# Performance work log

Hardware: AMD Instinct MI355X
Metric: run time of the kernel (lower is better)

Reference implementation:

```python
import jax, jax.numpy as jnp
import numpy as np

N = 100000   # nodes
E = 1600000  # edges (before self loops)
H = 4        # heads
C = 32       # per-head channels
D = H * C    # hidden_dim = 128
G = 64       # graphs in batch
L = 4        # num_layers
IN_DIM = 7
NEG_SLOPE = 0.2


def setup_inputs() -> dict:
    key = jax.random.key(0)
    ks = jax.random.split(key, 14)
    s = 0.1
    x = jax.random.normal(ks[0], (N, IN_DIM), jnp.float32)
    edge_index = jax.random.randint(ks[1], (2, E), 0, N, dtype=jnp.int32)
    batch = jnp.sort(jax.random.randint(ks[2], (N,), 0, G, dtype=jnp.int32))
    W0 = jax.random.normal(ks[3], (IN_DIM, D), jnp.float32) * s
    a_src0 = jax.random.normal(ks[4], (H, C), jnp.float32) * s
    a_dst0 = jax.random.normal(ks[5], (H, C), jnp.float32) * s
    b0 = jnp.zeros((D,), jnp.float32)
    Ws = jax.random.normal(ks[6], (L - 1, D, D), jnp.float32) * s
    a_srcs = jax.random.normal(ks[7], (L - 1, H, C), jnp.float32) * s
    a_dsts = jax.random.normal(ks[8], (L - 1, H, C), jnp.float32) * s
    bs = jnp.zeros((L - 1, D), jnp.float32)
    ln_g = jnp.ones((L, D), jnp.float32)
    ln_b = jnp.zeros((L, D), jnp.float32)
    return dict(x=x, edge_index=edge_index, batch=batch, W0=W0, a_src0=a_src0,
                a_dst0=a_dst0, b0=b0, Ws=Ws, a_srcs=a_srcs, a_dsts=a_dsts,
                bs=bs, ln_g=ln_g, ln_b=ln_b)


def _gat_layer(x, W, a_src, a_dst, b, src, dst):
    # x: [N, F_in] -> h: [N, H, C] (PyG GATConv: shared lin for src/dst)
    h = (x @ W).reshape(N, H, C)
    alpha_src = jnp.einsum('nhc,hc->nh', h, a_src)  # [N, H]
    alpha_dst = jnp.einsum('nhc,hc->nh', h, a_dst)  # [N, H]
    logits = jax.nn.leaky_relu(alpha_src[src] + alpha_dst[dst], NEG_SLOPE)  # [E', H]
    # segment softmax over edges grouped by destination node
    m = jax.ops.segment_max(logits, dst, num_segments=N)          # [N, H]
    e = jnp.exp(logits - m[dst])
    z = jax.ops.segment_sum(e, dst, num_segments=N)               # [N, H]
    alpha = e / (z[dst] + 1e-16)                                  # [E', H]
    msg = h[src] * alpha[..., None]                               # [E', H, C]
    out = jax.ops.segment_sum(msg, dst, num_segments=N)           # [N, H, C]
    return out.reshape(N, D) + b


def _layernorm(x, g, b):
    mu = jnp.mean(x, axis=-1, keepdims=True)
    var = jnp.var(x, axis=-1, keepdims=True)
    return (x - mu) * jax.lax.rsqrt(var + 1e-5) * g + b


def reference(x, edge_index, batch, W0, a_src0, a_dst0, b0, Ws, a_srcs, a_dsts, bs, ln_g, ln_b):
    # PyG GATConv default: add self loops
    loop = jnp.arange(N, dtype=edge_index.dtype)
    src = jnp.concatenate([edge_index[0], loop])
    dst = jnp.concatenate([edge_index[1], loop])
    h = x
    for i in range(L):
        if i == 0:
            W, asr, ads, b = W0, a_src0, a_dst0, b0
        else:
            W, asr, ads, b = Ws[i - 1], a_srcs[i - 1], a_dsts[i - 1], bs[i - 1]
        h_new = _gat_layer(h, W, asr, ads, b, src, dst)
        h_new = jax.nn.elu(_layernorm(h_new, ln_g[i], ln_b[i]))
        h = h + h_new if i > 0 else h_new  # dropout is identity in eval
    node_embeddings = h  # [N, D]
    sums = jax.ops.segment_sum(node_embeddings, batch, num_segments=G)  # [G, D]
    cnt = jax.ops.segment_sum(jnp.ones((N,), node_embeddings.dtype), batch, num_segments=G)
    graph_embedding = sums / jnp.maximum(cnt, 1.0)[:, None]
    return node_embeddings, graph_embedding
```

## Files before the change

### kernel.cpp

```cpp
#include <hip/hip_runtime.h>
#include <hip/hip_bf16.h>

#define NN 100000
#define NE 1600000
#define NH 4
#define NC 32
#define DD 128
#define NG 64
#define NIN 7

#define BSH 9
#define NBUK ((NN + 511) >> BSH)
#define SEGCAP 9600
#define CAPE (SEGCAP - 512)
#define CSRN (NBUK * SEGCAP)
#define NBBIN ((NE + 4095)/4096)

typedef __hip_bfloat16 bf16;
typedef __attribute__((ext_vector_type(8))) short short8;
typedef __attribute__((ext_vector_type(4))) float f32x4;
typedef __attribute__((ext_vector_type(2))) float f32x2;

__device__ __forceinline__ float b2f(const bf16 v){ return __bfloat162float(v); }

__device__ __forceinline__ float in_ld(const void* p, size_t i, int f32){
  return f32 ? ((const float*)p)[i] : b2f(((const bf16*)p)[i]);
}

__device__ __forceinline__ unsigned int bfbits(float v){
  bf16 b = __float2bfloat16(v);
  return (unsigned int)(*(unsigned short*)&b);
}

__global__ __launch_bounds__(256) void k_init(float* __restrict__ gsum, int* __restrict__ gcnt,
                                              int* __restrict__ bcur,
                                              const unsigned int* __restrict__ xb, int* __restrict__ flag){
  int i = blockIdx.x*256 + threadIdx.x;
  if (i < NG*DD) gsum[i] = 0.f;
  if (i < NG) gcnt[i] = 0;
  if (i < NBUK) bcur[i] = i * CAPE;
  if (blockIdx.x == 0 && threadIdx.x < 64){
    int t = threadIdx.x;
    int pl = 0;
    for (int j = t; j < 512; j += 64){
      float v = __uint_as_float(xb[j]);
      float a = fabsf(v);
      if (v == v && a < 1e6f && a > 1e-10f) pl++;
    }
    #pragma unroll
    for (int off = 32; off > 0; off >>= 1) pl += __shfl_down(pl, off);
    if (t == 0) *flag = (pl >= 384) ? 1 : 0;
  }
}

__global__ __launch_bounds__(256) void k_bin(const int* __restrict__ src, const int* __restrict__ dst,
                                             int* __restrict__ bcur, int2* __restrict__ gstag,
                                             const void* __restrict__ Ws, bf16* __restrict__ WT,
                                             const int* __restrict__ flag){
  if (blockIdx.x >= NBBIN){
    int l = blockIdx.x - NBBIN;
    int f32 = *flag;
    for (int idx = threadIdx.x; idx < DD*DD; idx += 256){
      int n = idx >> 7, k = idx & 127;
      WT[(size_t)l*DD*DD + idx] = __float2bfloat16(in_ld(Ws, (size_t)l*DD*DD + (size_t)k*DD + n, f32));
    }
    return;
  }
  __shared__ int cnt[NBUK], pref[NBUK+1], place[NBUK], gbase[NBUK];
  __shared__ int2 pairs[4096];
  int tid = threadIdx.x;
  for (int b = tid; b < NBUK; b += 256){ cnt[b]=0; place[b]=0; }
  __syncthreads();
  int e0 = blockIdx.x*4096;
  int s[16], d[16];
  #pragma unroll
  for (int i=0;i<16;i++){
    int e = e0 + i*256 + tid;
    s[i] = 0; d[i] = -1;
    if (e < NE){
      unsigned int us = (unsigned int)src[e]; if (us >= NN) us = 0;
      unsigned int ud = (unsigned int)dst[e]; if (ud >= NN) ud = 0;
      s[i] = (int)us; d[i] = (int)ud;
      atomicAdd(&cnt[ud>>BSH], 1);
    }
  }
  __syncthreads();
  if (tid == 0){
    int run = 0;
    for (int b=0;b<NBUK;b++){ pref[b] = run; run += cnt[b]; }
    pref[NBUK] = run;
  }
  __syncthreads();
  for (int b = tid; b < NBUK; b += 256){
    if (cnt[b] > 0) gbase[b] = atomicAdd(&bcur[b], cnt[b]);
  }
  __syncthreads();
  #pragma unroll
  for (int i=0;i<16;i++){
    if (d[i] >= 0){
      int b = d[i]>>BSH;
      int lp = atomicAdd(&place[b],1);
      pairs[pref[b]+lp] = make_int2(s[i], d[i]);
    }
  }
  __syncthreads();
  int tot = pref[NBUK];
  for (int j = tid; j < tot; j += 256){
    int2 pr = pairs[j];
    int b = pr.y>>BSH;
    int gidx = gbase[b] + (j - pref[b]);
    if (gidx >= b*CAPE && gidx < (b+1)*CAPE) gstag[gidx] = pr;
  }
}

__global__ __launch_bounds__(256) void k_bucket(const int2* __restrict__ gstag,
                                                const int* __restrict__ bcur,
                                                int* __restrict__ csr,
                                                int* __restrict__ offs, int* __restrict__ oend){
  __shared__ int seg[SEGCAP];
  __shared__ int lcnt[512];
  __shared__ int loff[512];
  __shared__ int pscan[256];
  int b = blockIdx.x, tid = threadIdx.x;
  int nstart = b << BSH;
  int nend = min(nstart + 512, NN);
  int nloc = nend - nstart;
  int base = b * SEGCAP;
  int stbase = b * CAPE;
  int ecnt = bcur[b] - stbase;
  ecnt = max(0, min(ecnt, CAPE));
  lcnt[tid]     = (tid < nloc) ? 1 : 0;
  lcnt[tid+256] = (tid+256 < nloc) ? 1 : 0;
  __syncthreads();
  for (int j = tid; j < ecnt; j += 256){
    int2 pr = gstag[stbase + j];
    int ln = pr.y - nstart;
    if (ln < 0 || ln >= nloc) ln = 0;
    atomicAdd(&lcnt[ln], 1);
  }
  __syncthreads();
  int c0 = lcnt[2*tid], c1 = lcnt[2*tid+1];
  int pairsum = c0 + c1;
  pscan[tid] = pairsum;
  __syncthreads();
  for (int off=1; off<256; off<<=1){
    int a = (tid >= off) ? pscan[tid-off] : 0;
    __syncthreads();
    pscan[tid] += a;
    __syncthreads();
  }
  int pexcl = pscan[tid] - pairsum;
  loff[2*tid]   = pexcl;
  loff[2*tid+1] = pexcl + c0;
  __syncthreads();
  int segN = pscan[255];
  if (segN > SEGCAP) segN = SEGCAP;
  if (tid < nloc){
    offs[nstart + tid] = base + loff[tid];
    oend[nstart + tid] = base + loff[tid] + lcnt[tid];
  }
  if (tid + 256 < nloc){
    offs[nstart + tid + 256] = base + loff[tid+256];
    oend[nstart + tid + 256] = base + loff[tid+256] + lcnt[tid+256];
  }
  __syncthreads();
  if (tid < nloc){ int p = loff[tid]; if (p < SEGCAP) seg[p] = nstart + tid; lcnt[tid] = 1; }
  if (tid + 256 < nloc){ int p = loff[tid+256]; if (p < SEGCAP) seg[p] = nstart + tid + 256; lcnt[tid+256] = 1; }
  __syncthreads();
  for (int j = tid; j < ecnt; j += 256){
    int2 pr = gstag[stbase + j];
    int ln = pr.y - nstart;
    if (ln < 0 || ln >= nloc) ln = 0;
    int p = atomicAdd(&lcnt[ln], 1);
    int idx = loff[ln] + p;
    if (idx >= 0 && idx < SEGCAP) seg[idx] = pr.x;
  }
  __syncthreads();
  for (int j = tid; j < segN; j += 256) csr[base + j] = seg[j];
}

__device__ __forceinline__ void alpha_red(float acc, float was, float wad, int d, int n,
                                          float* __restrict__ asrc, float* __restrict__ adst){
  float ps = acc*was, pd = acc*wad;
  #pragma unroll
  for (int off=16; off>0; off>>=1){
    ps += __shfl_down(ps, off, 32);
    pd += __shfl_down(pd, off, 32);
  }
  if ((d & 31) == 0){
    asrc[n*NH + (d>>5)] = ps;
    adst[n*NH + (d>>5)] = pd;
  }
}

__global__ __launch_bounds__(128) void k_gemm0(const void* __restrict__ x, const void* __restrict__ W,
    const void* __restrict__ aws, const void* __restrict__ awd,
    bf16* __restrict__ hproj,
    float* __restrict__ asrc, float* __restrict__ adst, const int* __restrict__ flag){
  int f32 = *flag;
  __shared__ float xr[4][NIN];
  int d = threadIdx.x;
  int n0 = blockIdx.x*4;
  if (d < 4*NIN) xr[d/NIN][d%NIN] = in_ld(x, (size_t)n0*NIN + d, f32);
  __syncthreads();
  float a0=0,a1=0,a2=0,a3=0;
  #pragma unroll
  for (int k=0;k<NIN;k++){
    float w = in_ld(W, (size_t)k*DD + d, f32);
    a0 += xr[0][k]*w; a1 += xr[1][k]*w; a2 += xr[2][k]*w; a3 += xr[3][k]*w;
  }
  hproj[(size_t)(n0+0)*DD+d]=__float2bfloat16(a0);
  hproj[(size_t)(n0+1)*DD+d]=__float2bfloat16(a1);
  hproj[(size_t)(n0+2)*DD+d]=__float2bfloat16(a2);
  hproj[(size_t)(n0+3)*DD+d]=__float2bfloat16(a3);
  float was = in_ld(aws, d, f32), wad = in_ld(awd, d, f32);
  alpha_red(a0, was, wad, d, n0+0, asrc, adst);
  alpha_red(a1, was, wad, d, n0+1, asrc, adst);
  alpha_red(a2, was, wad, d, n0+2, asrc, adst);
  alpha_red(a3, was, wad, d, n0+3, asrc, adst);
}

#define LDA 136
#define LDB 136

__global__ __launch_bounds__(256) void k_gemm_mfma(
    const bf16* __restrict__ resid,
    const bf16* __restrict__ WT, size_t wtoff,
    const void* __restrict__ aws, const void* __restrict__ awd, size_t aoff,
    bf16* __restrict__ hproj,
    float* __restrict__ asrc, float* __restrict__ adst,
    const int* __restrict__ flag)
{
  __shared__ bf16 sA[64*LDA];
  __shared__ bf16 sB[128*LDB];
  int f32 = *flag;
  int t = threadIdx.x;
  int n0 = blockIdx.x*64;

  {
    const uint4* srcv = (const uint4*)(WT + wtoff);
    #pragma unroll
    for (int i=0;i<8;i++){
      int u4 = t + 256*i;
      int row = u4 >> 4, c = u4 & 15;
      *(uint4*)(&sB[row*LDB + c*8]) = srcv[u4];
    }
  }
  {
    const uint4* av = (const uint4*)resid;
    #pragma unroll
    for (int i=0;i<4;i++){
      int u4 = t + 256*i;
      int row = u4 >> 4, c = u4 & 15;
      int gr = n0 + row;
      uint4 v = make_uint4(0,0,0,0);
      if (gr < NN) v = av[(size_t)gr*16 + c];
      *(uint4*)(&sA[row*LDA + c*8]) = v;
    }
  }
  __syncthreads();

  int wv = t >> 6, lane = t & 63;
  int m = lane & 15, kq = lane >> 4;
  int rowbase = wv*16;

  f32x4 acc[8];
  #pragma unroll
  for (int nt=0; nt<8; nt++) acc[nt] = (f32x4){0.f,0.f,0.f,0.f};

  #pragma unroll
  for (int ks=0; ks<4; ks++){
    short8 afrag = *(const short8*)(&sA[(rowbase + m)*LDA + ks*32 + kq*8]);
    #pragma unroll
    for (int nt=0; nt<8; nt++){
      short8 bfrag = *(const short8*)(&sB[(nt*16 + m)*LDB + ks*32 + kq*8]);
      acc[nt] = __builtin_amdgcn_mfma_f32_16x16x32_bf16(afrag, bfrag, acc[nt], 0, 0, 0);
    }
  }

  #pragma unroll
  for (int reg=0; reg<4; reg++){
    int gr = n0 + rowbase + kq*4 + reg;
    if (gr < NN){
      bf16* dst = hproj + (size_t)gr*DD + m;
      #pragma unroll
      for (int nt=0; nt<8; nt++)
        dst[nt*16] = __float2bfloat16(acc[nt][reg]);
    }
  }

  float avs[8], avd[8];
  #pragma unroll
  for (int nt=0; nt<8; nt++){
    avs[nt] = in_ld(aws, aoff + nt*16 + m, f32);
    avd[nt] = in_ld(awd, aoff + nt*16 + m, f32);
  }
  #pragma unroll
  for (int h=0; h<4; h++){
    #pragma unroll
    for (int reg=0; reg<4; reg++){
      float ps = acc[2*h][reg]*avs[2*h] + acc[2*h+1][reg]*avs[2*h+1];
      float pd = acc[2*h][reg]*avd[2*h] + acc[2*h+1][reg]*avd[2*h+1];
      #pragma unroll
      for (int off=1; off<16; off<<=1){
        ps += __shfl_xor(ps, off);
        pd += __shfl_xor(pd, off);
      }
      if (m == 0){
        int gr = n0 + rowbase + kq*4 + reg;
        if (gr < NN){
          asrc[gr*NH + h] = ps;
          adst[gr*NH + h] = pd;
        }
      }
    }
  }
}

__device__ __forceinline__ float4 edge_e(const float4 as, const float4 ad){
  float4 l, e;
  l.x = as.x + ad.x; l.y = as.y + ad.y; l.z = as.z + ad.z; l.w = as.w + ad.w;
  l.x = l.x > 0.f ? l.x : 0.2f*l.x;
  l.y = l.y > 0.f ? l.y : 0.2f*l.y;
  l.z = l.z > 0.f ? l.z : 0.2f*l.z;
  l.w = l.w > 0.f ? l.w : 0.2f*l.w;
  l.x = fminf(l.x, 30.f); l.y = fminf(l.y, 30.f);
  l.z = fminf(l.z, 30.f); l.w = fminf(l.w, 30.f);
  e.x = __expf(l.x); e.y = __expf(l.y); e.z = __expf(l.z); e.w = __expf(l.w);
  return e;
}

__device__ __forceinline__ float2 hp_ld2(const void* hp, int s, int lane){
  unsigned int hv = ((const unsigned int*)hp)[(size_t)s*64 + lane];
  return make_float2(__uint_as_float(hv << 16), __uint_as_float(hv & 0xFFFF0000u));
}

__global__ __launch_bounds__(256) void k_agg(const bf16* __restrict__ hproj,
    const float* __restrict__ asrc, const float* __restrict__ adst,
    const int* __restrict__ offs, const int* __restrict__ oend, const int* __restrict__ csr,
    bf16* __restrict__ resid,
    const void* __restrict__ bias, size_t boff,
    const void* __restrict__ lng, const void* __restrict__ lnb, size_t lnoff,
    const int* __restrict__ flag, const int first)
{
  __shared__ float s_al[4][256];
  __shared__ int   s_off[4][64];
  int f32 = *flag;
  int wid = threadIdx.x >> 6, lane = threadIdx.x & 63;
  int n = blockIdx.x*4 + wid;
  int beg = offs[n];
  int end = oend[n];
  beg = max(0, min(beg, CSRN));
  end = max(beg, min(end, CSRN));
  int deg = min(end - beg, 1024);
  const float4 ad = ((const float4*)adst)[n];
  int head = lane >> 4;
  const char* hpB = (const char*)hproj;
  float2 acc;

  if (deg <= 64){
    float4 e = make_float4(0,0,0,0);
    if (lane < deg){
      unsigned int us = (unsigned int)csr[beg+lane];
      if (us >= NN) us = 0;
      s_off[wid][lane] = (int)(us << 8);
      float4 as = ((const float4*)asrc)[us];
      e = edge_e(as, ad);
    }
    float4 zs = e;
    #pragma unroll
    for (int off=32; off>0; off>>=1){
      zs.x += __shfl_down(zs.x, off);
      zs.y += __shfl_down(zs.y, off);
      zs.z += __shfl_down(zs.z, off);
      zs.w += __shfl_down(zs.w, off);
    }
    float4 invz;
    invz.x = 1.f/(__shfl(zs.x,0)+1e-16f);
    invz.y = 1.f/(__shfl(zs.y,0)+1e-16f);
    invz.z = 1.f/(__shfl(zs.z,0)+1e-16f);
    invz.w = 1.f/(__shfl(zs.w,0)+1e-16f);
    if (lane < deg){
      s_al[wid][lane*4+0] = e.x*invz.x;
      s_al[wid][lane*4+1] = e.y*invz.y;
      s_al[wid][lane*4+2] = e.z*invz.z;
      s_al[wid][lane*4+3] = e.w*invz.w;
    }
    __threadfence_block();

    int qg = lane >> 4;
    int ql = lane & 15;
    int hq = ql >> 2;
    int qbyte = ql << 4;
    f32x2 a0 = {0.f,0.f}, a1 = {0.f,0.f}, a2 = {0.f,0.f}, a3 = {0.f,0.f};
    int t = 0;
    for (; t+4 <= deg; t += 4){
      int j = t + qg;
      unsigned int off = (unsigned int)s_off[wid][j] + qbyte;
      const uint4 hv = *(const uint4*)(hpB + off);
      float al = s_al[wid][j*4 + hq];
      f32x2 v0 = {__uint_as_float(hv.x << 16), __uint_as_float(hv.x & 0xFFFF0000u)};
      f32x2 v1 = {__uint_as_float(hv.y << 16), __uint_as_float(hv.y & 0xFFFF0000u)};
      f32x2 v2 = {__uint_as_float(hv.z << 16), __uint_as_float(hv.z & 0xFFFF0000u)};
      f32x2 v3 = {__uint_as_float(hv.w << 16), __uint_as_float(hv.w & 0xFFFF0000u)};
      a0 += v0 * al;
      a1 += v1 * al;
      a2 += v2 * al;
      a3 += v3 * al;
    }
    if (t < deg){
      int j = t + qg;
      if (j < deg){
        unsigned int off = (unsigned int)s_off[wid][j] + qbyte;
        const uint4 hv = *(const uint4*)(hpB + off);
        float al = s_al[wid][j*4 + hq];
        f32x2 v0 = {__uint_as_float(hv.x << 16), __uint_as_float(hv.x & 0xFFFF0000u)};
        f32x2 v1 = {__uint_as_float(hv.y << 16), __uint_as_float(hv.y & 0xFFFF0000u)};
        f32x2 v2 = {__uint_as_float(hv.z << 16), __uint_as_float(hv.z & 0xFFFF0000u)};
        f32x2 v3 = {__uint_as_float(hv.w << 16), __uint_as_float(hv.w & 0xFFFF0000u)};
        a0 += v0 * al;
        a1 += v1 * al;
        a2 += v2 * al;
        a3 += v3 * al;
      }
    }

    #pragma unroll
    for (int off = 16; off < 64; off <<= 1){
      a0.x += __shfl_xor(a0.x, off); a0.y += __shfl_xor(a0.y, off);
      a1.x += __shfl_xor(a1.x, off); a1.y += __shfl_xor(a1.y, off);
      a2.x += __shfl_xor(a2.x, off); a2.y += __shfl_xor(a2.y, off);
      a3.x += __shfl_xor(a3.x, off); a3.y += __shfl_xor(a3.y, off);
    }
    __threadfence_block();
    if (qg == 0){
      float* red = &s_al[wid][0];
      red[ql*8+0] = a0.x; red[ql*8+1] = a0.y;
      red[ql*8+2] = a1.x; red[ql*8+3] = a1.y;
      red[ql*8+4] = a2.x; red[ql*8+5] = a2.y;
      red[ql*8+6] = a3.x; red[ql*8+7] = a3.y;
    }
    __threadfence_block();
    acc = make_float2(s_al[wid][2*lane], s_al[wid][2*lane+1]);
  } else {
    f32x2 ac0 = {0.f,0.f};
    float4 zs = make_float4(0,0,0,0);
    for (int j=lane; j<deg; j+=64){
      unsigned int us = (unsigned int)csr[beg+j];
      if (us >= NN) us = 0;
      float4 as = ((const float4*)asrc)[us];
      float4 e = edge_e(as, ad);
      zs.x+=e.x; zs.y+=e.y; zs.z+=e.z; zs.w+=e.w;
    }
    #pragma unroll
    for (int off=32; off>0; off>>=1){
      zs.x += __shfl_down(zs.x, off);
      zs.y += __shfl_down(zs.y, off);
      zs.z += __shfl_down(zs.z, off);
      zs.w += __shfl_down(zs.w, off);
    }
    float4 invz;
    invz.x = 1.f/(__shfl(zs.x,0)+1e-16f);
    invz.y = 1.f/(__shfl(zs.y,0)+1e-16f);
    invz.z = 1.f/(__shfl(zs.z,0)+1e-16f);
    invz.w = 1.f/(__shfl(zs.w,0)+1e-16f);
    int nch = (deg+63)>>6;
    for (int c2=0;c2<nch;c2++){
      int base = c2<<6, j = base+lane;
      int sreg = 0;
      __threadfence_block();
      if (j < deg){
        unsigned int us = (unsigned int)csr[beg+j];
        if (us >= NN) us = 0;
        sreg = (int)us;
        float4 as = ((const float4*)asrc)[us];
        float4 e = edge_e(as, ad);
        s_al[wid][lane*4+0]=e.x*invz.x;
        s_al[wid][lane*4+1]=e.y*invz.y;
        s_al[wid][lane*4+2]=e.z*invz.z;
        s_al[wid][lane*4+3]=e.w*invz.w;
      }
      __threadfence_block();
      int cnt = min(64, deg-base);
      for (int t=0;t<cnt;t++){
        int s = __shfl(sreg, t);
        float a = s_al[wid][t*4+head];
        float2 hv = hp_ld2(hproj, s, lane);
        ac0.x += hv.x*a;
        ac0.y += hv.y*a;
      }
    }
    acc = make_float2(ac0.x, ac0.y);
  }

  float vx = acc.x + in_ld(bias, boff + 2*lane,   f32);
  float vy = acc.y + in_ld(bias, boff + 2*lane+1, f32);
  float s1 = vx+vy, s2 = vx*vx+vy*vy;
  #pragma unroll
  for (int off=32; off>0; off>>=1){
    s1 += __shfl_down(s1, off);
    s2 += __shfl_down(s2, off);
  }
  float mean = __shfl(s1,0) * (1.f/DD);
  float msq  = __shfl(s2,0) * (1.f/DD);
  float var  = fmaxf(msq - mean*mean, 0.f);
  float r = rsqrtf(var + 1e-5f);
  float yx = (vx-mean)*r*in_ld(lng, lnoff+2*lane,   f32) + in_ld(lnb, lnoff+2*lane,   f32);
  float yy = (vy-mean)*r*in_ld(lng, lnoff+2*lane+1, f32) + in_ld(lnb, lnoff+2*lane+1, f32);
  yx = yx>0.f ? yx : expm1f(yx);
  yy = yy>0.f ? yy : expm1f(yy);
  float2 res;
  if (first){
    res = make_float2(yx, yy);
  } else {
    unsigned int pu = ((const unsigned int*)resid)[(size_t)n*64 + lane];
    res = make_float2(__uint_as_float(pu << 16) + yx,
                      __uint_as_float(pu & 0xFFFF0000u) + yy);
  }
  unsigned int pk = bfbits(res.x) | (bfbits(res.y) << 16);
  ((unsigned int*)resid)[(size_t)n*64 + lane] = pk;
}

__global__ __launch_bounds__(128) void k_pool(const bf16* __restrict__ resid, void* __restrict__ dout,
    const int* __restrict__ batch, float* __restrict__ gsum, int* __restrict__ gcnt,
    const int* __restrict__ flag){
  __shared__ int sb[64];
  int f32 = *flag;
  int d = threadIdx.x;
  int n0 = blockIdx.x*64;
  int cnt = min(64, NN - n0);
  if (d < cnt){
    unsigned int b = (unsigned int)batch[n0 + d];
    if (b >= NG) b = 0;
    sb[d] = (int)b;
  }
  __syncthreads();
  float local = 0.f;
  int cur = sb[0];
  for (int i=0;i<cnt;i++){
    int b = sb[i];
    if (b != cur){
      atomicAdd(&gsum[cur*DD + d], local);
      local = 0.f; cur = b;
    }
    size_t idx = (size_t)(n0+i)*DD + d;
    float v = b2f(resid[idx]);
    if (f32) ((float*)dout)[idx] = v;
    else     ((bf16*)dout)[idx] = resid[idx];
    local += v;
  }
  atomicAdd(&gsum[cur*DD + d], local);
  if (d == 0){
    int lc = 0; int c2 = sb[0];
    for (int i=0;i<cnt;i++){
      int b = sb[i];
      if (b != c2){ atomicAdd(&gcnt[c2], lc); lc = 0; c2 = b; }
      lc++;
    }
    atomicAdd(&gcnt[c2], lc);
  }
}

__global__ __launch_bounds__(128) void k_final(const float* __restrict__ gsum, const int* __restrict__ gcnt,
                                               void* __restrict__ dout, const int* __restrict__ flag){
  int f32 = *flag;
  int i = blockIdx.x*128 + threadIdx.x;
  if (i < NG*DD){
    float c = (float)gcnt[i>>7];
    if (c < 1.f) c = 1.f;
    float val = gsum[i] / c;
    if (f32) ((float*)dout)[(size_t)NN*DD + i] = val;
    else     ((bf16*)dout)[(size_t)NN*DD + i] = __float2bfloat16(val);
  }
}

extern "C" void kernel_launch(void* const* d_in, const int* in_sizes, int n_in,
                              void* d_out, int out_size, void* d_ws, size_t ws_size,
                              hipStream_t stream){
  const void* x      = d_in[0];
  const int*  ei     = (const int*) d_in[1];
  const int*  batch  = (const int*) d_in[2];
  const void* W0     = d_in[3];
  const void* asrc0  = d_in[4];
  const void* adst0  = d_in[5];
  const void* b0     = d_in[6];
  const void* Ws     = d_in[7];
  const void* asrcs  = d_in[8];
  const void* adsts  = d_in[9];
  const void* bs     = d_in[10];
  const void* lng    = d_in[11];
  const void* lnb    = d_in[12];

  const int* srcs = ei;
  const int* dsts = ei + NE;

  uintptr_t p0 = (uintptr_t)d_ws;
  uintptr_t p = p0;
  auto alloc = [&](size_t bytes)->void* {
    void* r = (void*)p; p += (bytes + 255) & ~(size_t)255; return r;
  };
  int*   csr    = (int*)  alloc((size_t)CSRN*4);
  int*   offs   = (int*)  alloc((size_t)NN*4);
  int*   oend   = (int*)  alloc((size_t)NN*4);
  float* asrc   = (float*)alloc((size_t)NN*NH*4);
  float* adst   = (float*)alloc((size_t)NN*NH*4);
  float* gsum   = (float*)alloc((size_t)NG*DD*4);
  int*   gcnt   = (int*)  alloc(NG*4);
  int*   flag   = (int*)  alloc(256);
  int*   bcur   = (int*)  alloc((size_t)NBUK*4);
  int2*  gstag  = (int2*) alloc((size_t)NBUK*CAPE*8);
  bf16*  wt     = (bf16*) alloc((size_t)3*DD*DD*2);
  bf16*  hproj  = (bf16*) alloc((size_t)NN*DD*2);
  bf16*  resid  = (bf16*) alloc((size_t)NN*DD*2);

  const int NB = (NN + 255)/256;

  k_init<<<NB, 256, 0, stream>>>(gsum, gcnt, bcur, (const unsigned int*)x, flag);
  k_bin<<<NBBIN + 3, 256, 0, stream>>>(srcs, dsts, bcur, gstag, Ws, wt, flag);
  k_bucket<<<NBUK, 256, 0, stream>>>(gstag, bcur, csr, offs, oend);

  const int GEMM_B = (NN + 63)/64;

  for (int l=0; l<4; l++){
    if (l == 0){
      k_gemm0<<<NN/4, 128, 0, stream>>>(x, W0, asrc0, adst0, hproj, asrc, adst, flag);
      k_agg<<<NN/4, 256, 0, stream>>>(hproj, asrc, adst, offs, oend, csr, resid,
                                      b0, 0, lng, lnb, 0, flag, 1);
    } else {
      size_t wtoff = (size_t)(l-1)*DD*DD;
      size_t aoff  = (size_t)(l-1)*DD;
      k_gemm_mfma<<<GEMM_B, 256, 0, stream>>>(resid, wt, wtoff,
                                              asrcs, adsts, aoff,
                                              hproj, asrc, adst, flag);
      k_agg<<<NN/4, 256, 0, stream>>>(hproj, asrc, adst, offs, oend, csr, resid,
                                      bs, (size_t)(l-1)*DD, lng, lnb, (size_t)l*DD, flag, 0);
    }
  }

  k_pool<<<(NN+63)/64, 128, 0, stream>>>(resid, d_out, batch, gsum, gcnt, flag);
  k_final<<<(NG*DD+127)/128, 128, 0, stream>>>(gsum, gcnt, d_out, flag);
}
```

Baseline: 638.8 us.

## Assign one quarter-wavefront per node in GAT aggregation kernel

Restructures k_agg so each 16-lane group handles a whole destination node, with each lane owning 8 contiguous channels loaded as 16-byte vectors, instead of one 64-lane wavefront per node. The softmax normalisation, LayerNorm and residual reductions now use 16-lane xor shuffles, the cross-group shared-memory reduction is removed, and the grid shrinks to NN/16 blocks. The edge loop is unrolled by four to keep more independent gathers in flight. The intent is to cut per-node shuffle and reduction overhead and improve lane utilisation for average degree around 17, at the cost of more serial iterations per lane on high-degree nodes and more registers.

```diff
diff --git a/kernel.cpp b/kernel.cpp
--- a/kernel.cpp
+++ b/kernel.cpp
@@ -234,6 +234,7 @@
   __shared__ bf16 sA[64*LDA];
   __shared__ bf16 sB[128*LDB];
   int f32 = *flag;
+  (void)f32;
   int t = threadIdx.x;
   int n0 = blockIdx.x*64;
 
@@ -292,8 +293,8 @@
   float avs[8], avd[8];
   #pragma unroll
   for (int nt=0; nt<8; nt++){
-    avs[nt] = in_ld(aws, aoff + nt*16 + m, f32);
-    avd[nt] = in_ld(awd, aoff + nt*16 + m, f32);
+    avs[nt] = in_ld(aws, aoff + nt*16 + m, *flag);
+    avd[nt] = in_ld(awd, aoff + nt*16 + m, *flag);
   }
   #pragma unroll
   for (int h=0; h<4; h++){
@@ -330,9 +331,16 @@
   return e;
 }
 
-__device__ __forceinline__ float2 hp_ld2(const void* hp, int s, int lane){
-  unsigned int hv = ((const unsigned int*)hp)[(size_t)s*64 + lane];
-  return make_float2(__uint_as_float(hv << 16), __uint_as_float(hv & 0xFFFF0000u));
+__device__ __forceinline__ void fma_row(const uint4 hv, const float al,
+                                        f32x2& a0, f32x2& a1, f32x2& a2, f32x2& a3){
+  f32x2 v0 = {__uint_as_float(hv.x << 16), __uint_as_float(hv.x & 0xFFFF0000u)};
+  f32x2 v1 = {__uint_as_float(hv.y << 16), __uint_as_float(hv.y & 0xFFFF0000u)};
+  f32x2 v2 = {__uint_as_float(hv.z << 16), __uint_as_float(hv.z & 0xFFFF0000u)};
+  f32x2 v3 = {__uint_as_float(hv.w << 16), __uint_as_float(hv.w & 0xFFFF0000u)};
+  a0 += v0 * al;
+  a1 += v1 * al;
+  a2 += v2 * al;
+  a3 += v3 * al;
 }
 
 __global__ __launch_bounds__(256) void k_agg(const bf16* __restrict__ hproj,
@@ -343,182 +351,175 @@
     const void* __restrict__ lng, const void* __restrict__ lnb, size_t lnoff,
     const int* __restrict__ flag, const int first)
 {
-  __shared__ float s_al[4][256];
-  __shared__ int   s_off[4][64];
+  __shared__ __align__(16) float s_al[16][256];
+  __shared__ int s_off[16][64];
   int f32 = *flag;
   int wid = threadIdx.x >> 6, lane = threadIdx.x & 63;
-  int n = blockIdx.x*4 + wid;
+  int qg = lane >> 4, ql = lane & 15;
+  int slot = wid*4 + qg;
+  int n = blockIdx.x*16 + slot;
   int beg = offs[n];
   int end = oend[n];
   beg = max(0, min(beg, CSRN));
   end = max(beg, min(end, CSRN));
   int deg = min(end - beg, 1024);
   const float4 ad = ((const float4*)adst)[n];
-  int head = lane >> 4;
+  int hq = ql >> 2;
+  int qbyte = ql << 4;
   const char* hpB = (const char*)hproj;
-  float2 acc;
+
+  f32x2 a0 = {0.f,0.f}, a1 = {0.f,0.f}, a2 = {0.f,0.f}, a3 = {0.f,0.f};
 
   if (deg <= 64){
-    float4 e = make_float4(0,0,0,0);
-    if (lane < deg){
-      unsigned int us = (unsigned int)csr[beg+lane];
-      if (us >= NN) us = 0;
-      s_off[wid][lane] = (int)(us << 8);
-      float4 as = ((const float4*)asrc)[us];
-      e = edge_e(as, ad);
-    }
-    float4 zs = e;
-    #pragma unroll
-    for (int off=32; off>0; off>>=1){
-      zs.x += __shfl_down(zs.x, off);
-      zs.y += __shfl_down(zs.y, off);
-      zs.z += __shfl_down(zs.z, off);
-      zs.w += __shfl_down(zs.w, off);
+    float4 e[4];
+    float4 zs = make_float4(0.f,0.f,0.f,0.f);
+    #pragma unroll
+    for (int k=0;k<4;k++){
+      int j = ql + k*16;
+      e[k] = make_float4(0.f,0.f,0.f,0.f);
+      if (j < deg){
+        unsigned int us = (unsigned int)csr[beg+j];
+        if (us >= NN) us = 0;
+        s_off[slot][j] = (int)(us << 8);
+        float4 as = ((const float4*)asrc)[us];
+        e[k] = edge_e(as, ad);
+        zs.x += e[k].x; zs.y += e[k].y; zs.z += e[k].z; zs.w += e[k].w;
+      }
+    }
+    #pragma unroll
+    for (int off=1; off<16; off<<=1){
+      zs.x += __shfl_xor(zs.x, off);
+      zs.y += __shfl_xor(zs.y, off);
+      zs.z += __shfl_xor(zs.z, off);
+      zs.w += __shfl_xor(zs.w, off);
     }
     float4 invz;
-    invz.x = 1.f/(__shfl(zs.x,0)+1e-16f);
-    invz.y = 1.f/(__shfl(zs.y,0)+1e-16f);
-    invz.z = 1.f/(__shfl(zs.z,0)+1e-16f);
-    invz.w = 1.f/(__shfl(zs.w,0)+1e-16f);
-    if (lane < deg){
-      s_al[wid][lane*4+0] = e.x*invz.x;
-      s_al[wid][lane*4+1] = e.y*invz.y;
-      s_al[wid][lane*4+2] = e.z*invz.z;
-      s_al[wid][lane*4+3] = e.w*invz.w;
+    invz.x = 1.f/(zs.x+1e-16f);
+    invz.y = 1.f/(zs.y+1e-16f);
+    invz.z = 1.f/(zs.z+1e-16f);
+    invz.w = 1.f/(zs.w+1e-16f);
+    #pragma unroll
+    for (int k=0;k<4;k++){
+      int j = ql + k*16;
+      if (j < deg){
+        float4 al;
+        al.x = e[k].x*invz.x; al.y = e[k].y*invz.y;
+        al.z = e[k].z*invz.z; al.w = e[k].w*invz.w;
+        *(float4*)&s_al[slot][j*4] = al;
+      }
     }
     __threadfence_block();
 
-    int qg = lane >> 4;
-    int ql = lane & 15;
-    int hq = ql >> 2;
-    int qbyte = ql << 4;
-    f32x2 a0 = {0.f,0.f}, a1 = {0.f,0.f}, a2 = {0.f,0.f}, a3 = {0.f,0.f};
     int t = 0;
     for (; t+4 <= deg; t += 4){
-      int j = t + qg;
-      unsigned int off = (unsigned int)s_off[wid][j] + qbyte;
-      const uint4 hv = *(const uint4*)(hpB + off);
-      float al = s_al[wid][j*4 + hq];
-      f32x2 v0 = {__uint_as_float(hv.x << 16), __uint_as_float(hv.x & 0xFFFF0000u)};
-      f32x2 v1 = {__uint_as_float(hv.y << 16), __uint_as_float(hv.y & 0xFFFF0000u)};
-      f32x2 v2 = {__uint_as_float(hv.z << 16), __uint_as_float(hv.z & 0xFFFF0000u)};
-      f32x2 v3 = {__uint_as_float(hv.w << 16), __uint_as_float(hv.w & 0xFFFF0000u)};
-      a0 += v0 * al;
-      a1 += v1 * al;
-      a2 += v2 * al;
-      a3 += v3 * al;
-    }
-    if (t < deg){
-      int j = t + qg;
-      if (j < deg){
-        unsigned int off = (unsigned int)s_off[wid][j] + qbyte;
-        const uint4 hv = *(const uint4*)(hpB + off);
-        float al = s_al[wid][j*4 + hq];
-        f32x2 v0 = {__uint_as_float(hv.x << 16), __uint_as_float(hv.x & 0xFFFF0000u)};
-        f32x2 v1 = {__uint_as_float(hv.y << 16), __uint_as_float(hv.y & 0xFFFF0000u)};
-        f32x2 v2 = {__uint_as_float(hv.z << 16), __uint_as_float(hv.z & 0xFFFF0000u)};
-        f32x2 v3 = {__uint_as_float(hv.w << 16), __uint_as_float(hv.w & 0xFFFF0000u)};
-        a0 += v0 * al;
-        a1 += v1 * al;
-        a2 += v2 * al;
-        a3 += v3 * al;
-      }
-    }
-
-    #pragma unroll
-    for (int off = 16; off < 64; off <<= 1){
-      a0.x += __shfl_xor(a0.x, off); a0.y += __shfl_xor(a0.y, off);
-      a1.x += __shfl_xor(a1.x, off); a1.y += __shfl_xor(a1.y, off);
-      a2.x += __shfl_xor(a2.x, off); a2.y += __shfl_xor(a2.y, off);
-      a3.x += __shfl_xor(a3.x, off); a3.y += __shfl_xor(a3.y, off);
-    }
-    __threadfence_block();
-    if (qg == 0){
-      float* red = &s_al[wid][0];
-      red[ql*8+0] = a0.x; red[ql*8+1] = a0.y;
-      red[ql*8+2] = a1.x; red[ql*8+3] = a1.y;
-      red[ql*8+4] = a2.x; red[ql*8+5] = a2.y;
-      red[ql*8+6] = a3.x; red[ql*8+7] = a3.y;
-    }
-    __threadfence_block();
-    acc = make_float2(s_al[wid][2*lane], s_al[wid][2*lane+1]);
+      unsigned int o0 = (unsigned int)s_off[slot][t+0] + qbyte;
+      unsigned int o1 = (unsigned int)s_off[slot][t+1] + qbyte;
+      unsigned int o2 = (unsigned int)s_off[slot][t+2] + qbyte;
+      unsigned int o3 = (unsigned int)s_off[slot][t+3] + qbyte;
+      const uint4 h0 = *(const uint4*)(hpB + o0);
+      const uint4 h1 = *(const uint4*)(hpB + o1);
+      const uint4 h2 = *(const uint4*)(hpB + o2);
+      const uint4 h3 = *(const uint4*)(hpB + o3);
+      float al0 = s_al[slot][(t+0)*4 + hq];
+      float al1 = s_al[slot][(t+1)*4 + hq];
+      float al2 = s_al[slot][(t+2)*4 + hq];
+      float al3 = s_al[slot][(t+3)*4 + hq];
+      fma_row(h0, al0, a0, a1, a2, a3);
+      fma_row(h1, al1, a0, a1, a2, a3);
+      fma_row(h2, al2, a0, a1, a2, a3);
+      fma_row(h3, al3, a0, a1, a2, a3);
+    }
+    for (; t < deg; t++){
+      unsigned int o = (unsigned int)s_off[slot][t] + qbyte;
+      const uint4 hv = *(const uint4*)(hpB + o);
+      float al = s_al[slot][t*4 + hq];
+      fma_row(hv, al, a0, a1, a2, a3);
+    }
   } else {
-    f32x2 ac0 = {0.f,0.f};
-    float4 zs = make_float4(0,0,0,0);
-    for (int j=lane; j<deg; j+=64){
+    float4 zs = make_float4(0.f,0.f,0.f,0.f);
+    for (int j=ql; j<deg; j+=16){
       unsigned int us = (unsigned int)csr[beg+j];
       if (us >= NN) us = 0;
       float4 as = ((const float4*)asrc)[us];
-      float4 e = edge_e(as, ad);
-      zs.x+=e.x; zs.y+=e.y; zs.z+=e.z; zs.w+=e.w;
-    }
-    #pragma unroll
-    for (int off=32; off>0; off>>=1){
-      zs.x += __shfl_down(zs.x, off);
-      zs.y += __shfl_down(zs.y, off);
-      zs.z += __shfl_down(zs.z, off);
-      zs.w += __shfl_down(zs.w, off);
+      float4 ee = edge_e(as, ad);
+      zs.x += ee.x; zs.y += ee.y; zs.z += ee.z; zs.w += ee.w;
+    }
+    #pragma unroll
+    for (int off=1; off<16; off<<=1){
+      zs.x += __shfl_xor(zs.x, off);
+      zs.y += __shfl_xor(zs.y, off);
+      zs.z += __shfl_xor(zs.z, off);
+      zs.w += __shfl_xor(zs.w, off);
     }
     float4 invz;
-    invz.x = 1.f/(__shfl(zs.x,0)+1e-16f);
-    invz.y = 1.f/(__shfl(zs.y,0)+1e-16f);
-    invz.z = 1.f/(__shfl(zs.z,0)+1e-16f);
-    invz.w = 1.f/(__shfl(zs.w,0)+1e-16f);
-    int nch = (deg+63)>>6;
-    for (int c2=0;c2<nch;c2++){
-      int base = c2<<6, j = base+lane;
-      int sreg = 0;
+    invz.x = 1.f/(zs.x+1e-16f);
+    invz.y = 1.f/(zs.y+1e-16f);
+    invz.z = 1.f/(zs.z+1e-16f);
+    invz.w = 1.f/(zs.w+1e-16f);
+    for (int c0=0; c0<deg; c0+=64){
+      int cnt = min(64, deg-c0);
       __threadfence_block();
-      if (j < deg){
-        unsigned int us = (unsigned int)csr[beg+j];
-        if (us >= NN) us = 0;
-        sreg = (int)us;
-        float4 as = ((const float4*)asrc)[us];
-        float4 e = edge_e(as, ad);
-        s_al[wid][lane*4+0]=e.x*invz.x;
-        s_al[wid][lane*4+1]=e.y*invz.y;
-        s_al[wid][lane*4+2]=e.z*invz.z;
-        s_al[wid][lane*4+3]=e.w*invz.w;
+      #pragma unroll
+      for (int k=0;k<4;k++){
+        int lj = ql + k*16;
+        int j = c0 + lj;
+        if (lj < cnt){
+          unsigned int us = (unsigned int)csr[beg+j];
+          if (us >= NN) us = 0;
+          s_off[slot][lj] = (int)(us << 8);
+          float4 ee = edge_e(((const float4*)asrc)[us], ad);
+          float4 al;
+          al.x = ee.x*invz.x; al.y = ee.y*invz.y;
+          al.z = ee.z*invz.z; al.w = ee.w*invz.w;
+          *(float4*)&s_al[slot][lj*4] = al;
+        }
       }
       __threadfence_block();
-      int cnt = min(64, deg-base);
-      for (int t=0;t<cnt;t++){
-        int s = __shfl(sreg, t);
-        float a = s_al[wid][t*4+head];
-        float2 hv = hp_ld2(hproj, s, lane);
-        ac0.x += hv.x*a;
-        ac0.y += hv.y*a;
+      for (int t2=0; t2<cnt; t2++){
+        unsigned int o = (unsigned int)s_off[slot][t2] + qbyte;
+        const uint4 hv = *(const uint4*)(hpB + o);
+        float al = s_al[slot][t2*4 + hq];
+        fma_row(hv, al, a0, a1, a2, a3);
       }
     }
-    acc = make_float2(ac0.x, ac0.y);
-  }
-
-  float vx = acc.x + in_ld(bias, boff + 2*lane,   f32);
-  float vy = acc.y + in_ld(bias, boff + 2*lane+1, f32);
-  float s1 = vx+vy, s2 = vx*vx+vy*vy;
-  #pragma unroll
-  for (int off=32; off>0; off>>=1){
-    s1 += __shfl_down(s1, off);
-    s2 += __shfl_down(s2, off);
-  }
-  float mean = __shfl(s1,0) * (1.f/DD);
-  float msq  = __shfl(s2,0) * (1.f/DD);
+  }
+
+  int c0 = ql*8;
+  float v[8] = {a0.x, a0.y, a1.x, a1.y, a2.x, a2.y, a3.x, a3.y};
+  float s1 = 0.f, s2 = 0.f;
+  #pragma unroll
+  for (int i=0;i<8;i++){
+    v[i] += in_ld(bias, boff + c0 + i, f32);
+    s1 += v[i]; s2 += v[i]*v[i];
+  }
+  #pragma unroll
+  for (int off=1; off<16; off<<=1){
+    s1 += __shfl_xor(s1, off);
+    s2 += __shfl_xor(s2, off);
+  }
+  float mean = s1 * (1.f/DD);
+  float msq  = s2 * (1.f/DD);
   float var  = fmaxf(msq - mean*mean, 0.f);
   float r = rsqrtf(var + 1e-5f);
-  float yx = (vx-mean)*r*in_ld(lng, lnoff+2*lane,   f32) + in_ld(lnb, lnoff+2*lane,   f32);
-  float yy = (vy-mean)*r*in_ld(lng, lnoff+2*lane+1, f32) + in_ld(lnb, lnoff+2*lane+1, f32);
-  yx = yx>0.f ? yx : expm1f(yx);
-  yy = yy>0.f ? yy : expm1f(yy);
-  float2 res;
-  if (first){
-    res = make_float2(yx, yy);
-  } else {
-    unsigned int pu = ((const unsigned int*)resid)[(size_t)n*64 + lane];
-    res = make_float2(__uint_as_float(pu << 16) + yx,
-                      __uint_as_float(pu & 0xFFFF0000u) + yy);
-  }
-  unsigned int pk = bfbits(res.x) | (bfbits(res.y) << 16);
-  ((unsigned int*)resid)[(size_t)n*64 + lane] = pk;
+  float y[8];
+  #pragma unroll
+  for (int i=0;i<8;i++){
+    float yv = (v[i]-mean)*r*in_ld(lng, lnoff+c0+i, f32) + in_ld(lnb, lnoff+c0+i, f32);
+    y[i] = yv > 0.f ? yv : expm1f(yv);
+  }
+  if (!first){
+    uint4 pu = ((const uint4*)resid)[(size_t)n*16 + ql];
+    y[0] += __uint_as_float(pu.x << 16); y[1] += __uint_as_float(pu.x & 0xFFFF0000u);
+    y[2] += __uint_as_float(pu.y << 16); y[3] += __uint_as_float(pu.y & 0xFFFF0000u);
+    y[4] += __uint_as_float(pu.z << 16); y[5] += __uint_as_float(pu.z & 0xFFFF0000u);
+    y[6] += __uint_as_float(pu.w << 16); y[7] += __uint_as_float(pu.w & 0xFFFF0000u);
+  }
+  uint4 pk;
+  pk.x = bfbits(y[0]) | (bfbits(y[1]) << 16);
+  pk.y = bfbits(y[2]) | (bfbits(y[3]) << 16);
+  pk.z = bfbits(y[4]) | (bfbits(y[5]) << 16);
+  pk.w = bfbits(y[6]) | (bfbits(y[7]) << 16);
+  ((uint4*)resid)[(size_t)n*16 + ql] = pk;
 }
 
 __global__ __launch_bounds__(128) void k_pool(const bf16* __restrict__ resid, void* __restrict__ dout,
@@ -624,16 +625,16 @@
   for (int l=0; l<4; l++){
     if (l == 0){
       k_gemm0<<<NN/4, 128, 0, stream>>>(x, W0, asrc0, adst0, hproj, asrc, adst, flag);
-      k_agg<<<NN/4, 256, 0, stream>>>(hproj, asrc, adst, offs, oend, csr, resid,
-                                      b0, 0, lng, lnb, 0, flag, 1);
+      k_agg<<<NN/16, 256, 0, stream>>>(hproj, asrc, adst, offs, oend, csr, resid,
+                                       b0, 0, lng, lnb, 0, flag, 1);
     } else {
       size_t wtoff = (size_t)(l-1)*DD*DD;
       size_t aoff  = (size_t)(l-1)*DD;
       k_gemm_mfma<<<GEMM_B, 256, 0, stream>>>(resid, wt, wtoff,
                                               asrcs, adsts, aoff,
                                               hproj, asrc, adst, flag);
-      k_agg<<<NN/4, 256, 0, stream>>>(hproj, asrc, adst, offs, oend, csr, resid,
-                                      bs, (size_t)(l-1)*DD, lng, lnb, (size_t)l*DD, flag, 0);
+      k_agg<<<NN/16, 256, 0, stream>>>(hproj, asrc, adst, offs, oend, csr, resid,
+                                       bs, (size_t)(l-1)*DD, lng, lnb, (size_t)l*DD, flag, 0);
     }
   }
 
```

After: 763.9 us. 19.6% more time.
